# Optimization experiments

Hardware: AMD Instinct MI355X
Metric: run time of the kernel (lower is better)

The kernel has to match this reference:

```python
import jax, jax.numpy as jnp
import numpy as np
import math

EMBED_DIM = 1024
NUM_HEADS = 16
DEPTH = 12
HEAD_DIM = EMBED_DIM // NUM_HEADS // 2  # 32
LAMBDA_INIT = 0.8 - 0.6 * math.exp(-0.3 * DEPTH)
SCALE = HEAD_DIM ** -0.5  # flash_attn default softmax scale
RMS_EPS = 1e-5
BATCH, SEQ = 2, 2048


def _freqs(seq_len):
    # angle = 1 / 10000 ** linspace(0, 1, head_dim//2); freqs = pos * angle
    angle = 1.0 / 10000.0 ** jnp.linspace(0.0, 1.0, HEAD_DIM // 2)
    idx = jnp.arange(seq_len, dtype=jnp.float32)
    f = idx[:, None] * angle[None, :]
    return jnp.cos(f), jnp.sin(f)


def _rope_interleaved(x, cos, sin):
    # x: (b, t, h, d); cos/sin: (t, d//2). Interleaved pairs (0,1),(2,3),...
    x1, x2 = x[..., 0::2], x[..., 1::2]
    c = cos[None, :, None, :]
    s = sin[None, :, None, :]
    o1 = x1 * c - x2 * s
    o2 = x1 * s + x2 * c
    return jnp.stack([o1, o2], axis=-1).reshape(x.shape)


def _forward(x, Wq, Wk, Wv, Wo, lambda_q1, lambda_k1, lambda_q2, lambda_k2, rms_weight):
    b, t, _ = x.shape
    q = (x @ Wq.T).reshape(b, t, 2 * NUM_HEADS, HEAD_DIM)
    k = (x @ Wk.T).reshape(b, t, 2 * NUM_HEADS, HEAD_DIM)
    v = (x @ Wv.T).reshape(b, t, NUM_HEADS, 2, HEAD_DIM)
    cos, sin = _freqs(t)
    q = _rope_interleaved(q, cos, sin)
    k = _rope_interleaved(k, cos, sin)
    # split the 2H axis into (H, 2): q1/q2 are even/odd sub-heads
    q = q.reshape(b, t, NUM_HEADS, 2, HEAD_DIM)
    k = k.reshape(b, t, NUM_HEADS, 2, HEAD_DIM)
    q1, q2 = q[..., 0, :], q[..., 1, :]
    k1, k2 = k[..., 0, :], k[..., 1, :]
    v12 = v.reshape(b, t, NUM_HEADS, 2 * HEAD_DIM)  # == concat(v1, v2) on last dim

    def attend(qh, kh):
        scores = jnp.einsum('bthd,bshd->bhts', qh, kh) * SCALE
        p = jax.nn.softmax(scores, axis=-1)  # non-causal, as in source
        return jnp.einsum('bhts,bshe->bthe', p, v12)  # (b, t, H, 2*hd)

    attn1 = attend(q1, k1)
    attn2 = attend(q2, k2)
    lam = (jnp.exp(jnp.sum(lambda_q1 * lambda_k1))
           - jnp.exp(jnp.sum(lambda_q2 * lambda_k2)) + LAMBDA_INIT)
    a = attn1 - lam * attn2
    # RMSNorm over last dim (2*head_dim) with affine weight
    a = a * jax.lax.rsqrt(jnp.mean(a * a, axis=-1, keepdims=True) + RMS_EPS) * rms_weight
    a = a * (1.0 - LAMBDA_INIT)
    a = a.reshape(b, t, NUM_HEADS * 2 * HEAD_DIM)
    return a @ Wo.T


def setup_inputs() -> dict:
    key = jax.random.key(0)
    ks = jax.random.split(key, 9)
    std = EMBED_DIM ** -0.5
    return {
        'x': jax.random.normal(ks[0], (BATCH, SEQ, EMBED_DIM), jnp.float32),
        'Wq': jax.random.normal(ks[1], (EMBED_DIM, EMBED_DIM), jnp.float32) * std,
        'Wk': jax.random.normal(ks[2], (EMBED_DIM, EMBED_DIM), jnp.float32) * std,
        'Wv': jax.random.normal(ks[3], (EMBED_DIM, EMBED_DIM), jnp.float32) * std,
        'Wo': jax.random.normal(ks[4], (EMBED_DIM, EMBED_DIM), jnp.float32) * std,
        'lambda_q1': jax.random.normal(ks[5], (HEAD_DIM,), jnp.float32) * 0.1,
        'lambda_k1': jax.random.normal(ks[6], (HEAD_DIM,), jnp.float32) * 0.1,
        'lambda_q2': jax.random.normal(ks[7], (HEAD_DIM,), jnp.float32) * 0.1,
        'lambda_k2': jax.random.normal(ks[8], (HEAD_DIM,), jnp.float32) * 0.1,
        'rms_weight': jnp.ones((2 * HEAD_DIM,), jnp.float32),
    }


def reference(x, Wq, Wk, Wv, Wo, lambda_q1, lambda_k1, lambda_q2, lambda_k2, rms_weight):
    return _forward(x, Wq, Wk, Wv, Wo, lambda_q1, lambda_k1, lambda_q2, lambda_k2, rms_weight)
```

## Files before the change

### kernel.cpp

```cpp
#include <hip/hip_runtime.h>
#include <stdint.h>

typedef unsigned short u16;
typedef __bf16 bf16x8 __attribute__((ext_vector_type(8)));
typedef float f32x4 __attribute__((ext_vector_type(4)));
typedef float f32x16 __attribute__((ext_vector_type(16)));

#define TOKENS 4096
#define SEQLEN 2048
#define EMB 1024
#define NHEADS 16

static constexpr float LAMBDA_INIT_F = 0.7836057665316245f;
static constexpr float ONE_MINUS_LI  = 0.21639423346837553f;
static constexpr float SCALE_F       = 0.17677669529663687f;
static constexpr float LOG2E_F       = 1.4426950408889634f;

__device__ __forceinline__ u16 f2bf(float f) {
  uint32_t u = __builtin_bit_cast(uint32_t, f);
  u += 0x7fffu + ((u >> 16) & 1u);
  return (u16)(u >> 16);
}
__device__ __forceinline__ float bf2f(u16 h) {
  uint32_t u = ((uint32_t)h) << 16;
  return __builtin_bit_cast(float, u);
}
__device__ __forceinline__ float fast_exp2(float x) {
#if __has_builtin(__builtin_amdgcn_exp2f)
  return __builtin_amdgcn_exp2f(x);
#else
  return exp2f(x);
#endif
}
__device__ __forceinline__ void async16(const void* g, void* l) {
  __builtin_amdgcn_global_load_lds((__attribute__((address_space(1))) void*)(g),
                                   (__attribute__((address_space(3))) void*)(l),
                                   16, 0, 0);
}
__device__ __forceinline__ f32x4 mfma16(uint4 a, uint4 b, f32x4 c) {
  return __builtin_amdgcn_mfma_f32_16x16x32_bf16(
      __builtin_bit_cast(bf16x8, a), __builtin_bit_cast(bf16x8, b), c, 0, 0, 0);
}
__device__ __forceinline__ f32x16 mfma32(uint4 a, uint4 b, f32x16 c) {
  return __builtin_amdgcn_mfma_f32_32x32x16_bf16(
      __builtin_bit_cast(bf16x8, a), __builtin_bit_cast(bf16x8, b), c, 0, 0, 0);
}

__global__ __launch_bounds__(256) void prep_kernel(
    const float* __restrict__ x,  const float* __restrict__ wq,
    const float* __restrict__ wk, const float* __restrict__ wv,
    const float* __restrict__ wo, const float* __restrict__ lq1,
    const float* __restrict__ lk1,const float* __restrict__ lq2,
    const float* __restrict__ lk2,
    u16* __restrict__ xb, u16* __restrict__ wqb, u16* __restrict__ wkb,
    u16* __restrict__ wvb, u16* __restrict__ wob, float* __restrict__ lam_out)
{
  int i0 = (blockIdx.x * 256 + threadIdx.x) * 4;
  const float* src; u16* dst; int j;
  if (i0 < 4194304)      { src = x;  dst = xb;  j = i0; }
  else if (i0 < 5242880) { src = wq; dst = wqb; j = i0 - 4194304; }
  else if (i0 < 6291456) { src = wk; dst = wkb; j = i0 - 5242880; }
  else if (i0 < 7340032) { src = wv; dst = wvb; j = i0 - 6291456; }
  else                   { src = wo; dst = wob; j = i0 - 7340032; }
  float4 v = *(const float4*)(src + j);
  uint2 pack;
  pack.x = (uint32_t)f2bf(v.x) | ((uint32_t)f2bf(v.y) << 16);
  pack.y = (uint32_t)f2bf(v.z) | ((uint32_t)f2bf(v.w) << 16);
  *(uint2*)(dst + j) = pack;

  if (blockIdx.x == 0 && threadIdx.x == 0) {
    float d1 = 0.f, d2 = 0.f;
    for (int i = 0; i < 32; ++i) { d1 += lq1[i] * lk1[i]; d2 += lq2[i] * lk2[i]; }
    *lam_out = expf(d1) - expf(d2) + LAMBDA_INIT_F;
  }
}

template <int MODE>
__device__ __forceinline__ void gemm_body(const u16* __restrict__ A,
                                          const u16* __restrict__ B,
                                          void* __restrict__ C)
{
  __shared__ u16 As[128 * 64];
  __shared__ u16 Bs[128 * 64];
  const int t = threadIdx.x;
  const int lane = t & 63, w = t >> 6;
  const int q4 = lane >> 4, lm = lane & 15;
  const int wr = w >> 1, wc = w & 1;
  const int bm = blockIdx.y * 128, bn = blockIdx.x * 128;

  f32x4 acc[4][4];
#pragma unroll
  for (int mi = 0; mi < 4; ++mi)
#pragma unroll
    for (int ni = 0; ni < 4; ++ni) acc[mi][ni] = (f32x4){0.f, 0.f, 0.f, 0.f};

  for (int kt = 0; kt < 16; ++kt) {
    const int k0 = kt * 64;
    __syncthreads();
#pragma unroll
    for (int ro = 0; ro < 4; ++ro) {
      int ft = ro * 256 + t;
      int row = ft >> 3;
      int col = (((ft & 7) ^ (row & 7)) << 3);
      async16(&A[(bm + row) * 1024 + k0 + col], &As[ft * 8]);
      async16(&B[(bn + row) * 1024 + k0 + col], &Bs[ft * 8]);
    }
    __syncthreads();
#pragma unroll
    for (int ks = 0; ks < 2; ++ks) {
      uint4 af[4], bf[4];
#pragma unroll
      for (int mi = 0; mi < 4; ++mi)
        af[mi] = *(const uint4*)&As[(wr * 64 + mi * 16 + lm) * 64 +
                                    (((ks * 4 + q4) ^ (lm & 7)) << 3)];
#pragma unroll
      for (int ni = 0; ni < 4; ++ni)
        bf[ni] = *(const uint4*)&Bs[(wc * 64 + ni * 16 + lm) * 64 +
                                    (((ks * 4 + q4) ^ (lm & 7)) << 3)];
#pragma unroll
      for (int mi = 0; mi < 4; ++mi)
#pragma unroll
        for (int ni = 0; ni < 4; ++ni)
          acc[mi][ni] = mfma16(af[mi], bf[ni], acc[mi][ni]);
    }
  }
#pragma unroll
  for (int mi = 0; mi < 4; ++mi)
#pragma unroll
    for (int ni = 0; ni < 4; ++ni) {
      if (MODE == 2) {
        int token0 = bm + wr * 64 + mi * 16 + q4 * 4;
        int col = bn + wc * 64 + ni * 16 + lm;
        int bb = token0 >> 11, key0 = token0 & 2047;
        int h = col >> 6, d = col & 63;
        ushort4 pk;
        pk.x = f2bf(acc[mi][ni][0]);
        pk.y = f2bf(acc[mi][ni][1]);
        pk.z = f2bf(acc[mi][ni][2]);
        pk.w = f2bf(acc[mi][ni][3]);
        *(ushort4*)((u16*)C + ((size_t)((bb * 16 + h) * 64 + d)) * 2048 + key0) = pk;
      } else {
#pragma unroll
        for (int r = 0; r < 4; ++r) {
          int row = bm + wr * 64 + mi * 16 + q4 * 4 + r;
          int col = bn + wc * 64 + ni * 16 + lm;
          if (MODE == 1) ((float*)C)[row * 1024 + col] = acc[mi][ni][r];
          else           ((u16*)C)[row * 1024 + col]   = f2bf(acc[mi][ni][r]);
        }
      }
    }
}

__global__ __launch_bounds__(256) void gemm_qkv_kernel(
    const u16* __restrict__ xb, const u16* __restrict__ wqb,
    const u16* __restrict__ wkb, const u16* __restrict__ wvb,
    u16* __restrict__ qb, u16* __restrict__ kb, u16* __restrict__ vtb)
{
  if (blockIdx.z == 0)      gemm_body<0>(xb, wqb, qb);
  else if (blockIdx.z == 1) gemm_body<0>(xb, wkb, kb);
  else                      gemm_body<2>(xb, wvb, vtb);
}

__global__ __launch_bounds__(256) void gemm_out_kernel(
    const u16* __restrict__ ab, const u16* __restrict__ wob,
    float* __restrict__ out)
{
  gemm_body<1>(ab, wob, out);
}

__global__ __launch_bounds__(256) void rope_kernel(u16* __restrict__ qb,
                                                   u16* __restrict__ kb)
{
  int p = blockIdx.x * 256 + threadIdx.x;
  int tok = p >> 9;
  int pc = p & 511;
  int j = pc & 15;
  int tpos = tok & (SEQLEN - 1);
  float ang = exp2f(-(float)j * 0.8858474919699633f);
  float f = (float)tpos * ang;
  float s, c;
  sincosf(f, &s, &c);
  u16* ptr = ((blockIdx.y == 0) ? qb : kb) + tok * 1024 + pc * 2;
  uint32_t u = *(const uint32_t*)ptr;
  float x1 = bf2f((u16)(u & 0xffff));
  float x2 = bf2f((u16)(u >> 16));
  float o1 = x1 * c - x2 * s;
  float o2 = x1 * s + x2 * c;
  if (blockIdx.y == 0) { o1 *= SCALE_F * LOG2E_F; o2 *= SCALE_F * LOG2E_F; }
  *(uint32_t*)ptr = (uint32_t)f2bf(o1) | ((uint32_t)f2bf(o2) << 16);
}

__global__ __launch_bounds__(256, 4) void attn_kernel(
    const u16* __restrict__ qb, const u16* __restrict__ kb,
    const u16* __restrict__ vtb, const float* __restrict__ lam_p,
    const float* __restrict__ rmsw, u16* __restrict__ ab)
{
  __shared__ u16 smem[8192];

  const int t = threadIdx.x;
  const int lane = t & 63, w = t >> 6;
  const int l5 = lane >> 5, lr = lane & 31;
  const int c = w >> 1, rg = w & 1;
  const bool hi = (l5 != 0);
  const int qt = blockIdx.x, h = blockIdx.y, b = blockIdx.z;
  const int tok0 = b * SEQLEN + qt * 64;
  const int hch = h * 64;

  const u16* kbase = kb + (size_t)(b * SEQLEN) * 1024 + hch;
  const u16* vbase = vtb + (size_t)((b * 16 + h) * 64) * 2048;

#pragma unroll
  for (int ro = 0; ro < 2; ++ro) {
    int ft = ro * 256 + t;
    int row = ft >> 3;
    int col = (((ft & 7) ^ (row & 7)) << 3);
    async16(&qb[(tok0 + row) * 1024 + hch + col], &smem[ft * 8]);
  }
  __syncthreads();
  uint4 qf[2];
#pragma unroll
  for (int kk = 0; kk < 2; ++kk)
    qf[kk] = *(const uint4*)&smem[(rg * 32 + lr) * 64 +
                                  (((c * 4 + kk * 2 + l5) ^ (lr & 7)) << 3)];

  f32x16 O[2];
#pragma unroll
  for (int db = 0; db < 2; ++db)
#pragma unroll
    for (int i = 0; i < 16; ++i) O[db][i] = 0.f;
  float rs = 0.f;

  for (int kv = 0; kv < SEQLEN; kv += 64) {
    __syncthreads();
#pragma unroll
    for (int ro = 0; ro < 2; ++ro) {
      int ft = ro * 256 + t;
      int row = ft >> 3;
      int col = (((ft & 7) ^ (row & 7)) << 3);
      async16(kbase + (kv + row) * 1024 + col, &smem[ft * 8]);
      async16(vbase + row * 2048 + kv + col, &smem[4096 + ft * 8]);
    }
    __syncthreads();

    uint4 vf[2][4];
#pragma unroll
    for (int db = 0; db < 2; ++db)
#pragma unroll
      for (int kc = 0; kc < 4; ++kc)
        vf[db][kc] = *(const uint4*)&smem[4096 + (db * 32 + lr) * 64 +
                                          (((kc * 2 + l5) ^ (lr & 7)) << 3)];

#pragma unroll
    for (int kb2 = 0; kb2 < 2; ++kb2) {
      f32x16 s;
#pragma unroll
      for (int i = 0; i < 16; ++i) s[i] = 0.f;
#pragma unroll
      for (int kk = 0; kk < 2; ++kk) {
        uint4 kf = *(const uint4*)&smem[(kb2 * 32 + lr) * 64 +
                                        (((c * 4 + kk * 2 + l5) ^ (lr & 7)) << 3)];
        s = mfma32(kf, qf[kk], s);
      }
      uint32_t pk[8];
      float rloc = 0.f;
#pragma unroll
      for (int g = 0; g < 4; ++g) {
        float e0 = fast_exp2(s[g * 4 + 0]);
        float e1 = fast_exp2(s[g * 4 + 1]);
        float e2 = fast_exp2(s[g * 4 + 2]);
        float e3 = fast_exp2(s[g * 4 + 3]);
        rloc += (e0 + e1) + (e2 + e3);
        pk[2 * g]     = __builtin_amdgcn_perm(__builtin_bit_cast(uint32_t, e1),
                                              __builtin_bit_cast(uint32_t, e0),
                                              0x07060302u);
        pk[2 * g + 1] = __builtin_amdgcn_perm(__builtin_bit_cast(uint32_t, e3),
                                              __builtin_bit_cast(uint32_t, e2),
                                              0x07060302u);
      }
      rs += rloc;
#pragma unroll
      for (int t2 = 0; t2 < 2; ++t2) {
        uint32_t s0 = hi ? pk[4 * t2]     : pk[4 * t2 + 2];
        uint32_t s1 = hi ? pk[4 * t2 + 1] : pk[4 * t2 + 3];
        uint32_t r0 = (uint32_t)__shfl_xor((int)s0, 32);
        uint32_t r1 = (uint32_t)__shfl_xor((int)s1, 32);
        uint4 bfr;
        bfr.x = hi ? r0 : pk[4 * t2];
        bfr.y = hi ? r1 : pk[4 * t2 + 1];
        bfr.z = hi ? pk[4 * t2 + 2] : r0;
        bfr.w = hi ? pk[4 * t2 + 3] : r1;
        O[0] = mfma32(vf[0][kb2 * 2 + t2], bfr, O[0]);
        O[1] = mfma32(vf[1][kb2 * 2 + t2], bfr, O[1]);
      }
    }
  }

  rs += __shfl_xor(rs, 32);
  const int row64 = rg * 32 + lr;
  float* ex = (float*)smem;
  __syncthreads();

  if (c == 1) {
    float inv2 = (*lam_p) / rs;
#pragma unroll
    for (int db = 0; db < 2; ++db)
#pragma unroll
      for (int g = 0; g < 4; ++g) {
        int d0 = db * 32 + 8 * g + 4 * l5;
        int ch = (d0 >> 2) ^ (lr & 7);
        float4 v;
        v.x = O[db][4 * g + 0] * inv2;
        v.y = O[db][4 * g + 1] * inv2;
        v.z = O[db][4 * g + 2] * inv2;
        v.w = O[db][4 * g + 3] * inv2;
        *(float4*)&ex[row64 * 64 + ch * 4] = v;
      }
  }
  __syncthreads();
  if (c == 0) {
    float inv1 = 1.f / rs;
    float4 a4[8];
    float ssq = 0.f;
#pragma unroll
    for (int db = 0; db < 2; ++db)
#pragma unroll
      for (int g = 0; g < 4; ++g) {
        int d0 = db * 32 + 8 * g + 4 * l5;
        int ch = (d0 >> 2) ^ (lr & 7);
        float4 o2 = *(const float4*)&ex[row64 * 64 + ch * 4];
        float4 v;
        v.x = O[db][4 * g + 0] * inv1 - o2.x;
        v.y = O[db][4 * g + 1] * inv1 - o2.y;
        v.z = O[db][4 * g + 2] * inv1 - o2.z;
        v.w = O[db][4 * g + 3] * inv1 - o2.w;
        ssq += v.x * v.x + v.y * v.y + v.z * v.z + v.w * v.w;
        a4[db * 4 + g] = v;
      }
    ssq += __shfl_xor(ssq, 32);
    float sc = rsqrtf(ssq * (1.f / 64.f) + 1e-5f) * ONE_MINUS_LI;
    const int rowg = tok0 + row64;
#pragma unroll
    for (int db = 0; db < 2; ++db)
#pragma unroll
      for (int g = 0; g < 4; ++g) {
        int d0 = db * 32 + 8 * g + 4 * l5;
        float4 wv = *(const float4*)&rmsw[d0];
        float4 v = a4[db * 4 + g];
        ushort4 pq;
        pq.x = f2bf(v.x * sc * wv.x);
        pq.y = f2bf(v.y * sc * wv.y);
        pq.z = f2bf(v.z * sc * wv.z);
        pq.w = f2bf(v.w * sc * wv.w);
        *(ushort4*)&ab[rowg * 1024 + hch + d0] = pq;
      }
  }
}

extern "C" void kernel_launch(void* const* d_in, const int* in_sizes, int n_in,
                              void* d_out, int out_size, void* d_ws, size_t ws_size,
                              hipStream_t stream)
{
  (void)in_sizes; (void)n_in; (void)out_size; (void)ws_size;
  const float* x    = (const float*)d_in[0];
  const float* Wq   = (const float*)d_in[1];
  const float* Wk   = (const float*)d_in[2];
  const float* Wv   = (const float*)d_in[3];
  const float* Wo   = (const float*)d_in[4];
  const float* lq1  = (const float*)d_in[5];
  const float* lk1  = (const float*)d_in[6];
  const float* lq2  = (const float*)d_in[7];
  const float* lk2  = (const float*)d_in[8];
  const float* rmsw = (const float*)d_in[9];
  float* out = (float*)d_out;

  char* ws = (char*)d_ws;
  u16* xb   = (u16*)(ws + 0);
  u16* wqb  = (u16*)(ws + 8388608);
  u16* wkb  = (u16*)(ws + 10485760);
  u16* wvb  = (u16*)(ws + 12582912);
  u16* wob  = (u16*)(ws + 14680064);
  u16* qb   = (u16*)(ws + 16777216);
  u16* kb   = (u16*)(ws + 25165824);
  u16* vtb  = (u16*)(ws + 33554432);
  u16* ab   = (u16*)(ws + 41943040);
  float* lam = (float*)(ws + 50331648);

  hipLaunchKernelGGL(prep_kernel, dim3(8192), dim3(256), 0, stream,
                     x, Wq, Wk, Wv, Wo, lq1, lk1, lq2, lk2,
                     xb, wqb, wkb, wvb, wob, lam);
  hipLaunchKernelGGL(gemm_qkv_kernel, dim3(8, 32, 3), dim3(256), 0, stream,
                     xb, wqb, wkb, wvb, qb, kb, vtb);
  hipLaunchKernelGGL(rope_kernel, dim3(8192, 2), dim3(256), 0, stream, qb, kb);
  hipLaunchKernelGGL(attn_kernel, dim3(32, 16, 2), dim3(256), 0, stream,
                     qb, kb, vtb, lam, rmsw, ab);
  hipLaunchKernelGGL(gemm_out_kernel, dim3(8, 32, 1), dim3(256), 0, stream,
                     ab, wob, out);
}
```

Baseline: 240.1 us.

## Fuse RoPE into QKV GEMM epilogue and retile output GEMM to 64x128

Applies interleaved RoPE (plus the Q softmax scale) inside the Q/K projection GEMM epilogue, using lane shuffles to fetch the pair partner and hardware sin/cos on range-reduced angles. This removes the separate rope kernel and its read-modify-write pass over Q and K. The output projection gets its own 64x128 tiled GEMM launched on twice as many blocks to improve CU occupancy. The risks are extra transcendental work in the epilogue and slightly different sin/cos accuracy.

```diff
diff --git a/kernel.cpp b/kernel.cpp
--- a/kernel.cpp
+++ b/kernel.cpp
@@ -15,6 +15,7 @@
 static constexpr float ONE_MINUS_LI  = 0.21639423346837553f;
 static constexpr float SCALE_F       = 0.17677669529663687f;
 static constexpr float LOG2E_F       = 1.4426950408889634f;
+static constexpr float INV2PI_F      = 0.15915494309189535f;
 
 __device__ __forceinline__ u16 f2bf(float f) {
   uint32_t u = __builtin_bit_cast(uint32_t, f);
@@ -124,31 +125,64 @@
           acc[mi][ni] = mfma16(af[mi], bf[ni], acc[mi][ni]);
     }
   }
-#pragma unroll
-  for (int mi = 0; mi < 4; ++mi)
-#pragma unroll
-    for (int ni = 0; ni < 4; ++ni) {
-      if (MODE == 2) {
-        int token0 = bm + wr * 64 + mi * 16 + q4 * 4;
-        int col = bn + wc * 64 + ni * 16 + lm;
-        int bb = token0 >> 11, key0 = token0 & 2047;
-        int h = col >> 6, d = col & 63;
-        ushort4 pk;
-        pk.x = f2bf(acc[mi][ni][0]);
-        pk.y = f2bf(acc[mi][ni][1]);
-        pk.z = f2bf(acc[mi][ni][2]);
-        pk.w = f2bf(acc[mi][ni][3]);
-        *(ushort4*)((u16*)C + ((size_t)((bb * 16 + h) * 64 + d)) * 2048 + key0) = pk;
-      } else {
-#pragma unroll
-        for (int r = 0; r < 4; ++r) {
-          int row = bm + wr * 64 + mi * 16 + q4 * 4 + r;
+
+  if (MODE == 0 || MODE == 3) {
+    float angrev[2];
+    angrev[0] = exp2f(-(float)(lm >> 1) * 0.8858474919699633f) * INV2PI_F;
+    angrev[1] = exp2f(-(float)(8 + (lm >> 1)) * 0.8858474919699633f) * INV2PI_F;
+    const bool oddc = (lm & 1);
+    const float qsc = (MODE == 0) ? (SCALE_F * LOG2E_F) : 1.f;
+#pragma unroll
+    for (int mi = 0; mi < 4; ++mi)
+#pragma unroll
+      for (int r = 0; r < 4; ++r) {
+        int row = bm + wr * 64 + mi * 16 + q4 * 4 + r;
+        float tf = (float)(row & (SEQLEN - 1));
+        float sv[2], cv[2];
+#pragma unroll
+        for (int p = 0; p < 2; ++p) {
+          float prod = tf * angrev[p];
+          float fr = prod - floorf(prod);
+          sv[p] = __builtin_amdgcn_sinf(fr);
+          cv[p] = __builtin_amdgcn_cosf(fr);
+        }
+#pragma unroll
+        for (int ni = 0; ni < 4; ++ni) {
+          float v = acc[mi][ni][r];
+          float pv = __shfl_xor(v, 1);
+          int p = ni & 1;
+          float o = oddc ? (pv * sv[p] + v * cv[p]) : (v * cv[p] - pv * sv[p]);
+          o *= qsc;
           int col = bn + wc * 64 + ni * 16 + lm;
-          if (MODE == 1) ((float*)C)[row * 1024 + col] = acc[mi][ni][r];
-          else           ((u16*)C)[row * 1024 + col]   = f2bf(acc[mi][ni][r]);
+          ((u16*)C)[row * 1024 + col] = f2bf(o);
         }
       }
-    }
+  } else {
+#pragma unroll
+    for (int mi = 0; mi < 4; ++mi)
+#pragma unroll
+      for (int ni = 0; ni < 4; ++ni) {
+        if (MODE == 2) {
+          int token0 = bm + wr * 64 + mi * 16 + q4 * 4;
+          int col = bn + wc * 64 + ni * 16 + lm;
+          int bb = token0 >> 11, key0 = token0 & 2047;
+          int h = col >> 6, d = col & 63;
+          ushort4 pk;
+          pk.x = f2bf(acc[mi][ni][0]);
+          pk.y = f2bf(acc[mi][ni][1]);
+          pk.z = f2bf(acc[mi][ni][2]);
+          pk.w = f2bf(acc[mi][ni][3]);
+          *(ushort4*)((u16*)C + ((size_t)((bb * 16 + h) * 64 + d)) * 2048 + key0) = pk;
+        } else {
+#pragma unroll
+          for (int r = 0; r < 4; ++r) {
+            int row = bm + wr * 64 + mi * 16 + q4 * 4 + r;
+            int col = bn + wc * 64 + ni * 16 + lm;
+            ((float*)C)[row * 1024 + col] = acc[mi][ni][r];
+          }
+        }
+      }
+  }
 }
 
 __global__ __launch_bounds__(256) void gemm_qkv_kernel(
@@ -157,37 +191,74 @@
     u16* __restrict__ qb, u16* __restrict__ kb, u16* __restrict__ vtb)
 {
   if (blockIdx.z == 0)      gemm_body<0>(xb, wqb, qb);
-  else if (blockIdx.z == 1) gemm_body<0>(xb, wkb, kb);
+  else if (blockIdx.z == 1) gemm_body<3>(xb, wkb, kb);
   else                      gemm_body<2>(xb, wvb, vtb);
 }
 
 __global__ __launch_bounds__(256) void gemm_out_kernel(
-    const u16* __restrict__ ab, const u16* __restrict__ wob,
-    float* __restrict__ out)
-{
-  gemm_body<1>(ab, wob, out);
-}
-
-__global__ __launch_bounds__(256) void rope_kernel(u16* __restrict__ qb,
-                                                   u16* __restrict__ kb)
-{
-  int p = blockIdx.x * 256 + threadIdx.x;
-  int tok = p >> 9;
-  int pc = p & 511;
-  int j = pc & 15;
-  int tpos = tok & (SEQLEN - 1);
-  float ang = exp2f(-(float)j * 0.8858474919699633f);
-  float f = (float)tpos * ang;
-  float s, c;
-  sincosf(f, &s, &c);
-  u16* ptr = ((blockIdx.y == 0) ? qb : kb) + tok * 1024 + pc * 2;
-  uint32_t u = *(const uint32_t*)ptr;
-  float x1 = bf2f((u16)(u & 0xffff));
-  float x2 = bf2f((u16)(u >> 16));
-  float o1 = x1 * c - x2 * s;
-  float o2 = x1 * s + x2 * c;
-  if (blockIdx.y == 0) { o1 *= SCALE_F * LOG2E_F; o2 *= SCALE_F * LOG2E_F; }
-  *(uint32_t*)ptr = (uint32_t)f2bf(o1) | ((uint32_t)f2bf(o2) << 16);
+    const u16* __restrict__ A, const u16* __restrict__ B,
+    float* __restrict__ C)
+{
+  __shared__ u16 As[64 * 64];
+  __shared__ u16 Bs[128 * 64];
+  const int t = threadIdx.x;
+  const int lane = t & 63, w = t >> 6;
+  const int q4 = lane >> 4, lm = lane & 15;
+  const int wr = w >> 1, wc = w & 1;
+  const int bm = blockIdx.y * 64, bn = blockIdx.x * 128;
+
+  f32x4 acc[2][4];
+#pragma unroll
+  for (int mi = 0; mi < 2; ++mi)
+#pragma unroll
+    for (int ni = 0; ni < 4; ++ni) acc[mi][ni] = (f32x4){0.f, 0.f, 0.f, 0.f};
+
+  for (int kt = 0; kt < 16; ++kt) {
+    const int k0 = kt * 64;
+    __syncthreads();
+#pragma unroll
+    for (int ro = 0; ro < 2; ++ro) {
+      int ft = ro * 256 + t;
+      int row = ft >> 3;
+      int col = (((ft & 7) ^ (row & 7)) << 3);
+      async16(&A[(bm + row) * 1024 + k0 + col], &As[ft * 8]);
+    }
+#pragma unroll
+    for (int ro = 0; ro < 4; ++ro) {
+      int ft = ro * 256 + t;
+      int row = ft >> 3;
+      int col = (((ft & 7) ^ (row & 7)) << 3);
+      async16(&B[(bn + row) * 1024 + k0 + col], &Bs[ft * 8]);
+    }
+    __syncthreads();
+#pragma unroll
+    for (int ks = 0; ks < 2; ++ks) {
+      uint4 af[2], bf[4];
+#pragma unroll
+      for (int mi = 0; mi < 2; ++mi)
+        af[mi] = *(const uint4*)&As[(wr * 32 + mi * 16 + lm) * 64 +
+                                    (((ks * 4 + q4) ^ (lm & 7)) << 3)];
+#pragma unroll
+      for (int ni = 0; ni < 4; ++ni)
+        bf[ni] = *(const uint4*)&Bs[(wc * 64 + ni * 16 + lm) * 64 +
+                                    (((ks * 4 + q4) ^ (lm & 7)) << 3)];
+#pragma unroll
+      for (int mi = 0; mi < 2; ++mi)
+#pragma unroll
+        for (int ni = 0; ni < 4; ++ni)
+          acc[mi][ni] = mfma16(af[mi], bf[ni], acc[mi][ni]);
+    }
+  }
+#pragma unroll
+  for (int mi = 0; mi < 2; ++mi)
+#pragma unroll
+    for (int ni = 0; ni < 4; ++ni)
+#pragma unroll
+      for (int r = 0; r < 4; ++r) {
+        int row = bm + wr * 32 + mi * 16 + q4 * 4 + r;
+        int col = bn + wc * 64 + ni * 16 + lm;
+        C[row * 1024 + col] = acc[mi][ni][r];
+      }
 }
 
 __global__ __launch_bounds__(256, 4) void attn_kernel(
@@ -390,9 +461,8 @@
                      xb, wqb, wkb, wvb, wob, lam);
   hipLaunchKernelGGL(gemm_qkv_kernel, dim3(8, 32, 3), dim3(256), 0, stream,
                      xb, wqb, wkb, wvb, qb, kb, vtb);
-  hipLaunchKernelGGL(rope_kernel, dim3(8192, 2), dim3(256), 0, stream, qb, kb);
   hipLaunchKernelGGL(attn_kernel, dim3(32, 16, 2), dim3(256), 0, stream,
                      qb, kb, vtb, lam, rmsw, ab);
-  hipLaunchKernelGGL(gemm_out_kernel, dim3(8, 32, 1), dim3(256), 0, stream,
+  hipLaunchKernelGGL(gemm_out_kernel, dim3(8, 64), dim3(256), 0, stream,
                      ab, wob, out);
 }
```

New measurement: 247.6 us. 3.1% more time.
